# Kernel optimization log

Hardware: AMD Instinct MI355X
Metric: run time of the kernel (lower is better)

## Reference

```python
import jax, jax.numpy as jnp
import numpy as np
from jax import lax

PATCH = 3  # match_patch_size
EPS = 1e-9
WEIGHT = 100.0


def _patches(fm, p):
    # fm: [1, C, H, W] -> sliding p x p patches with reflect pad -> [H*W, C*p*p]
    pad = (p - 1) // 2
    fm_pad = jnp.pad(fm, ((0, 0), (0, 0), (pad, pad), (pad, pad)), mode='reflect')
    pt = lax.conv_general_dilated_patches(fm_pad, (p, p), (1, 1), 'VALID')  # [1, C*p*p, H, W]
    _, cpp, H, W = pt.shape
    return pt.reshape(cpp, H * W).T  # [H*W, C*p*p]


def _match_fm(content_fm, style_fm, p):
    # normalized cross-correlation patch match; returns matched style fm [1,C,H,W]
    _, C, H, W = content_fm.shape
    cp = _patches(content_fm, p)           # [HW, Cpp]
    sp = _patches(style_fm, p)             # [HW, Cpp]
    cn = jnp.sqrt(jnp.sum(cp * cp, axis=1))  # [HW]
    sn = jnp.sqrt(jnp.sum(sp * sp, axis=1))  # [HW]
    score = cp @ sp.T                       # [HW, HW] dense correlation
    score = score / (cn[:, None] * sn[None, :] + EPS)
    idx = jnp.argmax(score, axis=1)         # best style location per content location
    y, x = idx // W, idx % W
    corr = style_fm[0, :, y, x]             # [HW, C] gather
    return corr.T.reshape(1, C, H, W)


def _gram(fm):
    # fm: [B, C, H, W] -> [B, C, C]
    B, C, H, W = fm.shape
    f = fm.reshape(B, C, H * W)
    return jnp.einsum('bcx,bdx->bcd', f, f)


def setup_inputs() -> dict:
    key = jax.random.key(0)
    k1, k2, k3, k4 = jax.random.split(key, 4)
    shape = (1, 256, 64, 64)
    return {
        'content_fm': jax.random.normal(k1, shape, dtype=jnp.float32),
        'style_fm': jax.random.normal(k2, shape, dtype=jnp.float32),
        'input_fm': jax.random.normal(k3, shape, dtype=jnp.float32),
        'mask': jax.random.uniform(k4, (1, 1, 64, 64), dtype=jnp.float32),
    }


def reference(content_fm, style_fm, input_fm, mask):
    mask_exp = jnp.broadcast_to(mask, content_fm.shape)
    msum = jnp.sum(mask_exp)
    # capture_style phase: patch match + masked target gram
    corr = _match_fm(content_fm, style_fm, PATCH)
    target = lax.stop_gradient(_gram(corr * mask_exp) / msum)
    # loss phase
    G = _gram(input_fm * mask_exp) / msum
    loss = jnp.mean((G - target) ** 2) * WEIGHT
    return loss
```

## Files before the change

### kernel.cpp

```cpp
#include <hip/hip_runtime.h>
#include <math.h>

#define C_CH 256
#define NPOS 4096
#define GSLICE 32
#define CHUNK 8
#define ENC 4112

typedef __bf16 bf16x8 __attribute__((ext_vector_type(8)));
typedef float  f32x4  __attribute__((ext_vector_type(4)));

__device__ __forceinline__ int reflect_idx(int p) {
    int s = p - 1;
    if (s < 0) s = -s;
    if (s > 63) s = 126 - s;
    return s;
}

__device__ __forceinline__ unsigned short f2bf(float x) {
    unsigned int u = __float_as_uint(x);
    unsigned int r = u + 0x7fffu + ((u >> 16) & 1u);
    return (unsigned short)(r >> 16);
}

__device__ __forceinline__ unsigned int fmono(float f) {
    unsigned int b = __float_as_uint(f);
    return (b & 0x80000000u) ? ~b : (b | 0x80000000u);
}

__device__ __forceinline__ void gload16(const void* g, void* l) {
    __builtin_amdgcn_global_load_lds(
        (const __attribute__((address_space(1))) unsigned int*)g,
        (__attribute__((address_space(3))) unsigned int*)l, 16, 0, 0);
}

__global__ void __launch_bounds__(256)
split_kernel(const float* __restrict__ content, const float* __restrict__ style,
             unsigned short* __restrict__ cTH, unsigned short* __restrict__ cTL,
             unsigned short* __restrict__ sTH, unsigned short* __restrict__ sTL,
             float* __restrict__ SSp) {
    __shared__ float tile[64][65];
    int t = threadIdx.x;

    if (blockIdx.z == 2) {
        int bi = blockIdx.y * 64 + blockIdx.x;
        if (bi >= 128) return;
        int pos = ((bi & 15) << 8) + t;
        int cg = bi >> 4;
        float s = 0.f;
        for (int c = cg * 32; c < cg * 32 + 32; ++c) {
            float v = style[(size_t)c * NPOS + pos];
            s += v * v;
        }
        SSp[cg * NPOS + pos] = s;
        return;
    }

    const float* src = blockIdx.z ? style : content;
    unsigned short* oH = blockIdx.z ? sTH : cTH;
    unsigned short* oL = blockIdx.z ? sTL : cTL;
    int p0 = blockIdx.x * 64, c0 = blockIdx.y * 64;
    int posl = t & 63;
    int p = p0 + posl;
    #pragma unroll
    for (int r = 0; r < 16; ++r) {
        int cl = (t >> 6) + r * 4;
        tile[posl][cl] = src[(size_t)(c0 + cl) * NPOS + p];
    }
    __syncthreads();
    int cl2 = t & 63;
    #pragma unroll
    for (int r = 0; r < 16; ++r) {
        int pl = (t >> 6) + r * 4;
        int pg = p0 + pl;
        float x = tile[pl][cl2];
        unsigned short h = f2bf(x);
        float hf = __uint_as_float((unsigned int)h << 16);
        unsigned short l = f2bf(x - hf);
        oH[(size_t)pg * C_CH + c0 + cl2] = h;
        oL[(size_t)pg * C_CH + c0 + cl2] = l;
    }
}

__global__ void __launch_bounds__(512, 4)
egemm_mfma(const unsigned short* __restrict__ AH, const unsigned short* __restrict__ AL,
           const unsigned short* __restrict__ BH, const unsigned short* __restrict__ BL,
           float* __restrict__ E,
           const float* __restrict__ SSp, float* __restrict__ rs,
           unsigned long long* __restrict__ PK, int nwg) {
    __shared__ short sm[32768];

    int orig = blockIdx.x;
    int t = threadIdx.x;

    if (orig < 8) {
        int j = (orig << 9) + t;
        int yj = j >> 6, xj = j & 63;
        float s = 0.f;
        #pragma unroll
        for (int kh = 0; kh < 3; ++kh) {
            int ry = reflect_idx(yj + kh);
            #pragma unroll
            for (int kw = 0; kw < 3; ++kw) {
                int p = ry * 64 + reflect_idx(xj + kw);
                #pragma unroll
                for (int part = 0; part < 8; ++part)
                    s += SSp[part * NPOS + p];
            }
        }
        rs[j] = 1.0f / sqrtf(s);
        PK[j] = 0ull;
        asm volatile("s_waitcnt vmcnt(0)" ::: "memory");
    }

    int q = nwg >> 3;
    int xcd = orig & 7, rank = orig >> 3;
    int L = xcd * q + rank;
    int by = L >> 5, bx = L & 31;

    int lane = t & 63, wv = t >> 6;
    int wr = wv >> 2, wc = wv & 3;
    int bm = by * 128, bn = bx * 128;
    int rowLoc = lane >> 2;
    int kc2 = (((lane & 3) ^ ((lane >> 3) & 3))) << 3;
    int krd = (((lane >> 4) ^ ((lane >> 1) & 3))) << 3;

    const unsigned short* mats[4] = {AH, AL, BH, BL};
    const unsigned short* M = mats[wv >> 1];
    int rbase = ((wv >> 1) >= 2 ? bn : bm) + (wv & 1) * 64;
    const unsigned short* gp[4];
    #pragma unroll
    for (int i = 0; i < 4; ++i)
        gp[i] = M + (size_t)(rbase + i * 16 + rowLoc) * C_CH + kc2;
    int ldst = wv * 2048;

    auto STAGE = [&](short* base, int koff) {
        #pragma unroll
        for (int i = 0; i < 4; ++i)
            gload16(gp[i] + koff, base + ldst + i * 512);
    };

    f32x4 acc[4][2];
    #pragma unroll
    for (int mt = 0; mt < 4; ++mt)
        #pragma unroll
        for (int nt = 0; nt < 2; ++nt)
            acc[mt][nt] = (f32x4){0.f, 0.f, 0.f, 0.f};

    STAGE(sm, 0);

    #pragma unroll
    for (int ks = 0; ks < 8; ++ks) {
        short* cb = sm + (ks & 1) * 16384;
        if (ks < 7) {
            STAGE(sm + ((ks + 1) & 1) * 16384, (ks + 1) * 32);
            asm volatile("s_waitcnt vmcnt(4)" ::: "memory");
        } else {
            asm volatile("s_waitcnt vmcnt(0)" ::: "memory");
        }
        __builtin_amdgcn_s_barrier();
        __builtin_amdgcn_sched_barrier(0);

        short* sAH = cb;
        short* sAL = cb + 4096;
        short* sBH = cb + 8192;
        short* sBL = cb + 12288;
        bf16x8 aH[4], aL[4], bH[2], bL[2];
        #pragma unroll
        for (int mt = 0; mt < 4; ++mt) {
            int off = (wr * 64 + mt * 16 + (lane & 15)) * 32 + krd;
            aH[mt] = *(const bf16x8*)(sAH + off);
            aL[mt] = *(const bf16x8*)(sAL + off);
        }
        #pragma unroll
        for (int nt = 0; nt < 2; ++nt) {
            int off = (wc * 32 + nt * 16 + (lane & 15)) * 32 + krd;
            bH[nt] = *(const bf16x8*)(sBH + off);
            bL[nt] = *(const bf16x8*)(sBL + off);
        }
        __builtin_amdgcn_s_setprio(1);
        #pragma unroll
        for (int mt = 0; mt < 4; ++mt)
            #pragma unroll
            for (int nt = 0; nt < 2; ++nt) {
                f32x4 c = acc[mt][nt];
                c = __builtin_amdgcn_mfma_f32_16x16x32_bf16(aH[mt], bH[nt], c, 0, 0, 0);
                c = __builtin_amdgcn_mfma_f32_16x16x32_bf16(aH[mt], bL[nt], c, 0, 0, 0);
                c = __builtin_amdgcn_mfma_f32_16x16x32_bf16(aL[mt], bH[nt], c, 0, 0, 0);
                acc[mt][nt] = c;
            }
        __builtin_amdgcn_s_setprio(0);

        asm volatile("s_waitcnt lgkmcnt(0)" ::: "memory");
        __builtin_amdgcn_s_barrier();
        __builtin_amdgcn_sched_barrier(0);
    }

    #pragma unroll
    for (int mt = 0; mt < 4; ++mt) {
        int row0 = bm + wr * 64 + mt * 16 + (lane >> 4) * 4;
        #pragma unroll
        for (int nt = 0; nt < 2; ++nt) {
            int col = bn + wc * 32 + nt * 16 + (lane & 15);
            #pragma unroll
            for (int r2 = 0; r2 < 4; ++r2)
                E[(size_t)(row0 + r2) * ENC + col] = acc[mt][nt][r2];
        }
    }
}

__global__ void __launch_bounds__(256)
score_argmax(const float* __restrict__ E, const float* __restrict__ rs,
             unsigned long long* __restrict__ PK) {
    __shared__ float T[3 * 66 * 68];
    __shared__ float sv[4][64];
    __shared__ int   sj[4][64];

    int bid = blockIdx.x;
    int d = bid & 63;
    int c = bid >> 6;
    int s0 = c * CHUNK;
    int t = threadIdx.x;
    int xi = t & 63, s2 = t >> 6, xj0 = s2 * 16;
    int rr = t >> 2;
    int j0 = (t & 3) << 4;

    auto STORESTRIP = [&](float* Tb, const float* w) {
        float* row = Tb + (rr + 1) * 68;
        #pragma unroll
        for (int q2 = 0; q2 < 16; ++q2) row[1 + j0 + q2] = w[q2];
        if (j0 == 0)  row[0]  = w[1];
        if (j0 == 48) row[65] = w[14];
        if (rr == 1 || rr == 62) {
            float* erow = Tb + (rr == 1 ? 0 : 65) * 68;
            #pragma unroll
            for (int q2 = 0; q2 < 16; ++q2) erow[1 + j0 + q2] = w[q2];
            if (j0 == 0)  erow[0]  = w[1];
            if (j0 == 48) erow[65] = w[14];
        }
    };
    auto LOADSTRIP = [&](float* Tb, int cy, int sy) {
        int cyr = reflect_idx(cy), syr = reflect_idx(sy);
        const float* Eb = E + (size_t)(cyr * 64 + rr) * ENC + syr * 64 + j0;
        float w[16];
        *(float4*)&w[0]  = *(const float4*)&Eb[0];
        *(float4*)&w[4]  = *(const float4*)&Eb[4];
        *(float4*)&w[8]  = *(const float4*)&Eb[8];
        *(float4*)&w[12] = *(const float4*)&Eb[12];
        STORESTRIP(Tb, w);
    };

    bool valid = false;
    float pfv[16];

    for (int s = s0; s < s0 + CHUNK; ++s) {
        int yjl = (s + d) & 63;

        if (!valid) {
            __syncthreads();
            for (int kh = 0; kh < 3; ++kh)
                LOADSTRIP(T + ((s + kh) % 3) * 4488, s + kh, yjl + kh);
            __syncthreads();
            valid = true;
        }

        int yjl_next = (s + 1 + d) & 63;
        bool pf = (s + 1 < s0 + CHUNK) && (yjl_next == yjl + 1);
        if (pf) {
            int cyr = reflect_idx(s + 3), syr = reflect_idx(yjl + 3);
            const float* Eb = E + (size_t)(cyr * 64 + rr) * ENC + syr * 64 + j0;
            *(float4*)&pfv[0]  = *(const float4*)&Eb[0];
            *(float4*)&pfv[4]  = *(const float4*)&Eb[4];
            *(float4*)&pfv[8]  = *(const float4*)&Eb[8];
            *(float4*)&pfv[12] = *(const float4*)&Eb[12];
        }

        float sc[16];
        #pragma unroll
        for (int q2 = 0; q2 < 16; ++q2) sc[q2] = 0.f;
        #pragma unroll
        for (int kh = 0; kh < 3; ++kh) {
            const float* Tk = T + ((s + kh) % 3) * 4488;
            #pragma unroll
            for (int kw = 0; kw < 3; ++kw) {
                const float* rp = Tk + (xi + kw) * 68 + xj0;
                float rw[18];
                *(float4*)&rw[0]  = *(const float4*)&rp[0];
                *(float4*)&rw[4]  = *(const float4*)&rp[4];
                *(float4*)&rw[8]  = *(const float4*)&rp[8];
                *(float4*)&rw[12] = *(const float4*)&rp[12];
                if (kw > 0) *(float2*)&rw[16] = *(const float2*)&rp[16];
                #pragma unroll
                for (int q2 = 0; q2 < 16; ++q2) sc[q2] += rw[kw + q2];
            }
        }

        int jbase = (yjl << 6) + xj0;
        float bv = -INFINITY; int bj = 0;
        #pragma unroll
        for (int q2 = 0; q2 < 16; ++q2) {
            float v = sc[q2] * rs[jbase + q2];
            if (v > bv) { bv = v; bj = jbase + q2; }
        }
        sv[s2][xi] = bv; sj[s2][xi] = bj;
        __syncthreads();
        if (s2 == 0) {
            #pragma unroll
            for (int u = 1; u < 4; ++u) {
                float ov = sv[u][xi]; int oj = sj[u][xi];
                if (ov > bv || (ov == bv && oj < bj)) { bv = ov; bj = oj; }
            }
            unsigned long long pk =
                ((unsigned long long)fmono(bv) << 32) | (unsigned int)(~bj);
            atomicMax(PK + (s << 6) + xi, pk);
        }

        if (pf) {
            __syncthreads();
            STORESTRIP(T + ((s + 3) % 3) * 4488, pfv);
            __syncthreads();
        } else {
            valid = false;
        }
    }
}

__global__ void __launch_bounds__(256)
build_xy_kernel(const float* __restrict__ input_fm,
                const float* __restrict__ style,
                const float* __restrict__ mask,
                const unsigned long long* __restrict__ PK,
                unsigned short* __restrict__ XmH, unsigned short* __restrict__ XmL,
                unsigned short* __restrict__ YmH, unsigned short* __restrict__ YmL,
                float* __restrict__ out) {
    if (blockIdx.x == 0 && threadIdx.x == 0) *out = 0.0f;
    int e4 = blockIdx.x * 256 + threadIdx.x;
    int c = e4 >> 10;
    int i0 = (e4 & 1023) << 2;
    int base = (c << 12) + i0;
    float4 inv = *(const float4*)&input_fm[base];
    float4 mv  = *(const float4*)&mask[i0];
    const float* sc = style + ((size_t)c << 12);
    float x[4], y[4];
    x[0] = inv.x * mv.x; x[1] = inv.y * mv.y; x[2] = inv.z * mv.z; x[3] = inv.w * mv.w;
    float mvv[4] = {mv.x, mv.y, mv.z, mv.w};
    #pragma unroll
    for (int k = 0; k < 4; ++k) {
        unsigned long long pk = PK[i0 + k];
        int j = (int)(~(unsigned int)(pk & 0xffffffffu));
        y[k] = sc[j] * mvv[k];
    }
    ushort4 xh, xl, yh, yl;
    #pragma unroll
    for (int j = 0; j < 4; ++j) {
        unsigned short h = f2bf(x[j]);
        float hf = __uint_as_float((unsigned int)h << 16);
        ((unsigned short*)&xh)[j] = h;
        ((unsigned short*)&xl)[j] = f2bf(x[j] - hf);
        unsigned short h2 = f2bf(y[j]);
        float hf2 = __uint_as_float((unsigned int)h2 << 16);
        ((unsigned short*)&yh)[j] = h2;
        ((unsigned short*)&yl)[j] = f2bf(y[j] - hf2);
    }
    *(ushort4*)&XmH[base] = xh;
    *(ushort4*)&XmL[base] = xl;
    *(ushort4*)&YmH[base] = yh;
    *(ushort4*)&YmL[base] = yl;
}

__global__ void __launch_bounds__(256)
gram_mfma(const unsigned short* __restrict__ XH, const unsigned short* __restrict__ XL,
          const unsigned short* __restrict__ YH, const unsigned short* __restrict__ YL,
          float* __restrict__ Dpart) {
    __shared__ short sm[32768];
    const int PI[10] = {0,0,0,0,1,1,1,2,2,3};
    const int PJ[10] = {0,1,2,3,1,2,3,2,3,3};
    int pr = blockIdx.x, sl = blockIdx.y;
    int ti = PI[pr], tj = PJ[pr];
    int c0 = ti * 64, d0 = tj * 64;
    int t = threadIdx.x, lane = t & 63, wv = t >> 6;
    int wr = wv >> 1, wc = wv & 1;
    int rowLoc = wv * 16 + (lane >> 2);
    int kc2 = (((lane & 3) ^ ((lane >> 3) & 3))) << 3;
    int krd = (((lane >> 4) ^ ((lane >> 1) & 3))) << 3;
    int posBase = sl * 128 + kc2;

    const unsigned short* g0 = XH + (size_t)(c0 + rowLoc) * NPOS + posBase;
    const unsigned short* g1 = XL + (size_t)(c0 + rowLoc) * NPOS + posBase;
    const unsigned short* g2 = XH + (size_t)(d0 + rowLoc) * NPOS + posBase;
    const unsigned short* g3 = XL + (size_t)(d0 + rowLoc) * NPOS + posBase;
    const unsigned short* g4 = YH + (size_t)(c0 + rowLoc) * NPOS + posBase;
    const unsigned short* g5 = YL + (size_t)(c0 + rowLoc) * NPOS + posBase;
    const unsigned short* g6 = YH + (size_t)(d0 + rowLoc) * NPOS + posBase;
    const unsigned short* g7 = YL + (size_t)(d0 + rowLoc) * NPOS + posBase;
    int lb = wv * 512;

    auto STAGE = [&](short* base, int koff) {
        gload16(g0 + koff, base + lb);
        gload16(g1 + koff, base + 2048 + lb);
        gload16(g2 + koff, base + 4096 + lb);
        gload16(g3 + koff, base + 6144 + lb);
        gload16(g4 + koff, base + 8192 + lb);
        gload16(g5 + koff, base + 10240 + lb);
        gload16(g6 + koff, base + 12288 + lb);
        gload16(g7 + koff, base + 14336 + lb);
    };

    f32x4 aX[2][2], aY[2][2];
    #pragma unroll
    for (int mt = 0; mt < 2; ++mt)
        #pragma unroll
        for (int nt = 0; nt < 2; ++nt) {
            aX[mt][nt] = (f32x4){0.f, 0.f, 0.f, 0.f};
            aY[mt][nt] = (f32x4){0.f, 0.f, 0.f, 0.f};
        }

    STAGE(sm, 0);

    #pragma unroll
    for (int ks = 0; ks < 4; ++ks) {
        short* cb = sm + (ks & 1) * 16384;
        if (ks < 3) {
            STAGE(sm + ((ks + 1) & 1) * 16384, (ks + 1) * 32);
            asm volatile("s_waitcnt vmcnt(8)" ::: "memory");
        } else {
            asm volatile("s_waitcnt vmcnt(0)" ::: "memory");
        }
        __builtin_amdgcn_s_barrier();
        __builtin_amdgcn_sched_barrier(0);

        bf16x8 xcH[2], xcL[2], xdH[2], xdL[2], ycH[2], ycL[2], ydH[2], ydL[2];
        #pragma unroll
        for (int mt = 0; mt < 2; ++mt) {
            int off = (wr * 32 + mt * 16 + (lane & 15)) * 32 + krd;
            xcH[mt] = *(const bf16x8*)(cb + off);
            xcL[mt] = *(const bf16x8*)(cb + 2048 + off);
            ycH[mt] = *(const bf16x8*)(cb + 8192 + off);
            ycL[mt] = *(const bf16x8*)(cb + 10240 + off);
        }
        #pragma unroll
        for (int nt = 0; nt < 2; ++nt) {
            int off = (wc * 32 + nt * 16 + (lane & 15)) * 32 + krd;
            xdH[nt] = *(const bf16x8*)(cb + 4096 + off);
            xdL[nt] = *(const bf16x8*)(cb + 6144 + off);
            ydH[nt] = *(const bf16x8*)(cb + 12288 + off);
            ydL[nt] = *(const bf16x8*)(cb + 14336 + off);
        }
        __builtin_amdgcn_s_setprio(1);
        #pragma unroll
        for (int mt = 0; mt < 2; ++mt)
            #pragma unroll
            for (int nt = 0; nt < 2; ++nt) {
                f32x4 cx = aX[mt][nt];
                cx = __builtin_amdgcn_mfma_f32_16x16x32_bf16(xcH[mt], xdH[nt], cx, 0, 0, 0);
                cx = __builtin_amdgcn_mfma_f32_16x16x32_bf16(xcH[mt], xdL[nt], cx, 0, 0, 0);
                cx = __builtin_amdgcn_mfma_f32_16x16x32_bf16(xcL[mt], xdH[nt], cx, 0, 0, 0);
                aX[mt][nt] = cx;
                f32x4 cy = aY[mt][nt];
                cy = __builtin_amdgcn_mfma_f32_16x16x32_bf16(ycH[mt], ydH[nt], cy, 0, 0, 0);
                cy = __builtin_amdgcn_mfma_f32_16x16x32_bf16(ycH[mt], ydL[nt], cy, 0, 0, 0);
                cy = __builtin_amdgcn_mfma_f32_16x16x32_bf16(ycL[mt], ydH[nt], cy, 0, 0, 0);
                aY[mt][nt] = cy;
            }
        __builtin_amdgcn_s_setprio(0);

        asm volatile("s_waitcnt lgkmcnt(0)" ::: "memory");
        __builtin_amdgcn_s_barrier();
        __builtin_amdgcn_sched_barrier(0);
    }

    float* fs = (float*)sm;
    #pragma unroll
    for (int mt = 0; mt < 2; ++mt) {
        int rl = wr * 32 + mt * 16 + ((lane >> 4) << 2);
        #pragma unroll
        for (int nt = 0; nt < 2; ++nt) {
            int cl = wc * 32 + nt * 16 + (lane & 15);
            #pragma unroll
            for (int r2 = 0; r2 < 4; ++r2)
                fs[(rl + r2) * 68 + cl] = aX[mt][nt][r2] - aY[mt][nt][r2];
        }
    }
    __syncthreads();
    float* Db = Dpart + ((size_t)sl * 10 + pr) * 4096;
    int rr0 = t >> 4;
    int cc0 = (t & 15) << 2;
    #pragma unroll
    for (int i = 0; i < 4; ++i) {
        int rr = rr0 + (i << 4);
        *(float4*)&Db[rr * 64 + cc0] = *(const float4*)&fs[rr * 68 + cc0];
    }
}

__global__ void __launch_bounds__(256)
loss_kernel(const float* __restrict__ Dpart, const float* __restrict__ mask,
            float* __restrict__ out) {
    const int PI[10] = {0,0,0,0,1,1,1,2,2,3};
    const int PJ[10] = {0,1,2,3,1,2,3,2,3,3};
    __shared__ float red[4];
    int tid = threadIdx.x;

    float ms = 0.f;
    for (int i = tid; i < NPOS; i += 256) ms += mask[i];
    #pragma unroll
    for (int o = 32; o >= 1; o >>= 1) ms += __shfl_down(ms, o, 64);
    if ((tid & 63) == 0) red[tid >> 6] = ms;
    __syncthreads();
    float msum = 256.0f * (red[0] + red[1] + red[2] + red[3]);
    __syncthreads();

    int e2 = blockIdx.x * 256 + tid;
    int tt = e2 >> 12;
    int ei = e2 & 4095;
    float d = 0.f;
    #pragma unroll
    for (int s = 0; s < GSLICE; ++s)
        d += Dpart[(size_t)(s * 10 + tt) * 4096 + ei];
    float inv = 1.0f / msum;
    float v = d * inv;
    float w = (PI[tt] != PJ[tt]) ? 2.0f : 1.0f;
    float ls = w * v * v;
    #pragma unroll
    for (int o = 32; o >= 1; o >>= 1) ls += __shfl_down(ls, o, 64);
    if ((tid & 63) == 0) red[tid >> 6] = ls;
    __syncthreads();
    if (tid == 0)
        atomicAdd(out, (red[0] + red[1] + red[2] + red[3]) * (100.0f / 65536.0f));
}

extern "C" void kernel_launch(void* const* d_in, const int* in_sizes, int n_in,
                              void* d_out, int out_size, void* d_ws, size_t ws_size,
                              hipStream_t stream) {
    (void)in_sizes; (void)n_in; (void)out_size; (void)ws_size;
    const float* content = (const float*)d_in[0];
    const float* style   = (const float*)d_in[1];
    const float* input   = (const float*)d_in[2];
    const float* mask    = (const float*)d_in[3];
    float* out = (float*)d_out;

    auto alignup = [](size_t b) { return (b + 255) & ~size_t(255); };
    char* ws = (char*)d_ws;
    size_t off = 0;
    auto alloc = [&](size_t bytes) { void* p = ws + off; off += alignup(bytes); return p; };

    unsigned short* cTH = (unsigned short*)alloc((size_t)NPOS * C_CH * 2);
    unsigned short* cTL = (unsigned short*)alloc((size_t)NPOS * C_CH * 2);
    unsigned short* sTH = (unsigned short*)alloc((size_t)NPOS * C_CH * 2);
    unsigned short* sTL = (unsigned short*)alloc((size_t)NPOS * C_CH * 2);
    float* SSp   = (float*)alloc((size_t)8 * NPOS * 4);
    float* rs    = (float*)alloc((size_t)NPOS * 4);
    unsigned long long* PK = (unsigned long long*)alloc((size_t)NPOS * 8);
    unsigned short* XmH = (unsigned short*)alloc((size_t)C_CH * NPOS * 2);
    unsigned short* XmL = (unsigned short*)alloc((size_t)C_CH * NPOS * 2);
    unsigned short* YmH = (unsigned short*)alloc((size_t)C_CH * NPOS * 2);
    unsigned short* YmL = (unsigned short*)alloc((size_t)C_CH * NPOS * 2);
    float* Dpart = (float*)alloc((size_t)GSLICE * 10 * 4096 * 4);
    float* E     = (float*)alloc((size_t)NPOS * ENC * 4);

    split_kernel<<<dim3(64, 4, 3), 256, 0, stream>>>(content, style, cTH, cTL, sTH, sTL, SSp);

    int nwg = 1024;
    egemm_mfma<<<nwg, 512, 0, stream>>>(cTH, cTL, sTH, sTL, E, SSp, rs, PK, nwg);
    score_argmax<<<512, 256, 0, stream>>>(E, rs, PK);
    build_xy_kernel<<<1024, 256, 0, stream>>>(input, style, mask, PK, XmH, XmL, YmH, YmL, out);
    gram_mfma<<<dim3(10, GSLICE), 256, 0, stream>>>(XmH, XmL, YmH, YmL, Dpart);
    loss_kernel<<<160, 256, 0, stream>>>(Dpart, mask, out);
}
```

Before: 101.7 us.

## Fuse loss reduction into gram kernel via atomic accumulation and last-block finish

Gram slices now accumulate their 64x64 partial differences into one shared buffer with float atomics, instead of writing 32 separate partial slices. A global counter picks the last finishing block, which computes the mask sum and the final loss itself. This removes the separate loss kernel launch and the round trip through the partial-slice buffer. In exchange it adds many contended global atomics and a serial single-block final reduction over 40960 elements, and the float atomic order makes the result nondeterministic.

```diff
diff --git a/kernel.cpp b/kernel.cpp
--- a/kernel.cpp
+++ b/kernel.cpp
@@ -332,9 +332,10 @@
                 const unsigned long long* __restrict__ PK,
                 unsigned short* __restrict__ XmH, unsigned short* __restrict__ XmL,
                 unsigned short* __restrict__ YmH, unsigned short* __restrict__ YmL,
-                float* __restrict__ out) {
-    if (blockIdx.x == 0 && threadIdx.x == 0) *out = 0.0f;
+                float* __restrict__ Gd) {
     int e4 = blockIdx.x * 256 + threadIdx.x;
+    if (e4 <= 10240)
+        *(float4*)&Gd[e4 << 2] = (float4){0.f, 0.f, 0.f, 0.f};
     int c = e4 >> 10;
     int i0 = (e4 & 1023) << 2;
     int base = (c << 12) + i0;
@@ -371,7 +372,8 @@
 __global__ void __launch_bounds__(256)
 gram_mfma(const unsigned short* __restrict__ XH, const unsigned short* __restrict__ XL,
           const unsigned short* __restrict__ YH, const unsigned short* __restrict__ YL,
-          float* __restrict__ Dpart) {
+          float* __restrict__ Gd, const float* __restrict__ mask,
+          float* __restrict__ out) {
     __shared__ short sm[32768];
     const int PI[10] = {0,0,0,0,1,1,1,2,2,3};
     const int PJ[10] = {0,1,2,3,1,2,3,2,3,3};
@@ -469,7 +471,7 @@
         __builtin_amdgcn_sched_barrier(0);
     }
 
-    float* fs = (float*)sm;
+    float* Gt = Gd + pr * 4096;
     #pragma unroll
     for (int mt = 0; mt < 2; ++mt) {
         int rl = wr * 32 + mt * 16 + ((lane >> 4) << 2);
@@ -478,54 +480,45 @@
             int cl = wc * 32 + nt * 16 + (lane & 15);
             #pragma unroll
             for (int r2 = 0; r2 < 4; ++r2)
-                fs[(rl + r2) * 68 + cl] = aX[mt][nt][r2] - aY[mt][nt][r2];
-        }
-    }
+                atomicAdd(&Gt[(rl + r2) * 64 + cl], aX[mt][nt][r2] - aY[mt][nt][r2]);
+        }
+    }
+
+    __threadfence();
+    int* flags = (int*)sm;
+    float* red = (float*)sm + 4;
     __syncthreads();
-    float* Db = Dpart + ((size_t)sl * 10 + pr) * 4096;
-    int rr0 = t >> 4;
-    int cc0 = (t & 15) << 2;
-    #pragma unroll
-    for (int i = 0; i < 4; ++i) {
-        int rr = rr0 + (i << 4);
-        *(float4*)&Db[rr * 64 + cc0] = *(const float4*)&fs[rr * 68 + cc0];
-    }
-}
-
-__global__ void __launch_bounds__(256)
-loss_kernel(const float* __restrict__ Dpart, const float* __restrict__ mask,
-            float* __restrict__ out) {
-    const int PI[10] = {0,0,0,0,1,1,1,2,2,3};
-    const int PJ[10] = {0,1,2,3,1,2,3,2,3,3};
-    __shared__ float red[4];
-    int tid = threadIdx.x;
+    if (t == 0) {
+        int old = atomicAdd((int*)(Gd + 40960), 1);
+        flags[0] = (old == 10 * GSLICE - 1);
+    }
+    __syncthreads();
+    if (!flags[0]) return;
 
     float ms = 0.f;
-    for (int i = tid; i < NPOS; i += 256) ms += mask[i];
+    for (int i = t; i < NPOS; i += 256) ms += mask[i];
     #pragma unroll
     for (int o = 32; o >= 1; o >>= 1) ms += __shfl_down(ms, o, 64);
-    if ((tid & 63) == 0) red[tid >> 6] = ms;
+    if ((t & 63) == 0) red[t >> 6] = ms;
     __syncthreads();
     float msum = 256.0f * (red[0] + red[1] + red[2] + red[3]);
+    float inv = 1.0f / msum;
     __syncthreads();
 
-    int e2 = blockIdx.x * 256 + tid;
-    int tt = e2 >> 12;
-    int ei = e2 & 4095;
-    float d = 0.f;
-    #pragma unroll
-    for (int s = 0; s < GSLICE; ++s)
-        d += Dpart[(size_t)(s * 10 + tt) * 4096 + ei];
-    float inv = 1.0f / msum;
-    float v = d * inv;
-    float w = (PI[tt] != PJ[tt]) ? 2.0f : 1.0f;
-    float ls = w * v * v;
+    float ls = 0.f;
+    for (int i = t; i < 40960; i += 256) {
+        float dv = __hip_atomic_load(&Gd[i], __ATOMIC_RELAXED, __HIP_MEMORY_SCOPE_AGENT);
+        int tt = i >> 12;
+        float w = (PI[tt] != PJ[tt]) ? 2.0f : 1.0f;
+        float v = dv * inv;
+        ls += w * v * v;
+    }
     #pragma unroll
     for (int o = 32; o >= 1; o >>= 1) ls += __shfl_down(ls, o, 64);
-    if ((tid & 63) == 0) red[tid >> 6] = ls;
+    if ((t & 63) == 0) red[t >> 6] = ls;
     __syncthreads();
-    if (tid == 0)
-        atomicAdd(out, (red[0] + red[1] + red[2] + red[3]) * (100.0f / 65536.0f));
+    if (t == 0)
+        *out = (red[0] + red[1] + red[2] + red[3]) * (100.0f / 65536.0f);
 }
 
 extern "C" void kernel_launch(void* const* d_in, const int* in_sizes, int n_in,
@@ -554,7 +547,7 @@
     unsigned short* XmL = (unsigned short*)alloc((size_t)C_CH * NPOS * 2);
     unsigned short* YmH = (unsigned short*)alloc((size_t)C_CH * NPOS * 2);
     unsigned short* YmL = (unsigned short*)alloc((size_t)C_CH * NPOS * 2);
-    float* Dpart = (float*)alloc((size_t)GSLICE * 10 * 4096 * 4);
+    float* Gd    = (float*)alloc((size_t)41216 * 4);
     float* E     = (float*)alloc((size_t)NPOS * ENC * 4);
 
     split_kernel<<<dim3(64, 4, 3), 256, 0, stream>>>(content, style, cTH, cTL, sTH, sTL, SSp);
@@ -562,7 +555,6 @@
     int nwg = 1024;
     egemm_mfma<<<nwg, 512, 0, stream>>>(cTH, cTL, sTH, sTL, E, SSp, rs, PK, nwg);
     score_argmax<<<512, 256, 0, stream>>>(E, rs, PK);
-    build_xy_kernel<<<1024, 256, 0, stream>>>(input, style, mask, PK, XmH, XmL, YmH, YmL, out);
-    gram_mfma<<<dim3(10, GSLICE), 256, 0, stream>>>(XmH, XmL, YmH, YmL, Dpart);
-    loss_kernel<<<160, 256, 0, stream>>>(Dpart, mask, out);
-}
+    build_xy_kernel<<<1024, 256, 0, stream>>>(input, style, mask, PK, XmH, XmL, YmH, YmL, Gd);
+    gram_mfma<<<dim3(10, GSLICE), 256, 0, stream>>>(XmH, XmL, YmH, YmL, Gd, mask, out);
+}
```

Result: slower. 167.4 us (+64.6%).
